# Kernel tuning notes

Hardware: AMD Instinct MI355X
Metric: run time of the kernel (lower is better)

Reference implementation:

```python
import jax, jax.numpy as jnp
import numpy as np

B, C, D, H, W = 2, 128, 32, 64, 64  # ch_in=128, shurink=0 -> Cs = ch_out = C
Cs = C


def setup_inputs() -> dict:
    key = jax.random.key(0)
    ks = jax.random.split(key, 9)
    std = 1.0 / np.sqrt(C).astype(np.float32)
    x = jax.random.normal(ks[0], (B, C, D, H, W), jnp.float32)
    Wk = jax.random.normal(ks[1], (Cs, C), jnp.float32) * std
    bk = jax.random.normal(ks[2], (Cs,), jnp.float32) * std
    Wq = jax.random.normal(ks[3], (Cs, C), jnp.float32) * std
    bq = jax.random.normal(ks[4], (Cs,), jnp.float32) * std
    Wv = jax.random.normal(ks[5], (Cs, C), jnp.float32) * std
    bv = jax.random.normal(ks[6], (Cs,), jnp.float32) * std
    Wo = jax.random.normal(ks[7], (C, Cs), jnp.float32) * (1.0 / np.sqrt(Cs).astype(np.float32))
    bo = jax.random.normal(ks[8], (C,), jnp.float32) * std
    return {"x": x, "Wk": Wk, "bk": bk, "Wq": Wq, "bq": bq, "Wv": Wv, "bv": bv, "Wo": Wo, "bo": bo}


def reference(x, Wk, bk, Wq, bq, Wv, bv, Wo, bo):
    # 1x1x1 Conv3d == per-voxel linear over channels
    def proj(Wt, bt):
        return jnp.einsum('bcdhw,oc->bodhw', x, Wt) + bt[None, :, None, None, None]

    K = proj(Wk, bk)  # [B,Cs,D,H,W]
    Q = proj(Wq, bq)
    V = proj(Wv, bv)

    scale = 1.0 / jnp.sqrt(jnp.asarray(Cs, x.dtype))
    # per-pixel depth attention: scores[b,h,w,i,j] = sum_c K[b,c,i,h,w] * Q[b,c,j,h,w]
    scores = jnp.einsum('bcihw,bcjhw->bhwij', K, Q) * scale
    # torch softmax dim=1 on [N,D,D] == key-position axis i (axis=-2 here)
    A = jax.nn.softmax(scores, axis=-2)
    # a[b,c,j,h,w] = sum_i V[b,c,i,h,w] * A[b,h,w,i,j]  (== bmm(V, A))
    a = jnp.einsum('bcihw,bhwij->bcjhw', V, A)
    out = jnp.einsum('bcjhw,oc->bojhw', a, Wo) + bo[None, :, None, None, None]
    return x + out  # atten_factor = 1
```

## Files before the change

kernel.cpp:

```cpp
#include <hip/hip_runtime.h>

typedef _Float16 f16x8 __attribute__((ext_vector_type(8)));
typedef _Float16 f16x4 __attribute__((ext_vector_type(4)));
typedef float    f32x4 __attribute__((ext_vector_type(4)));

#define MFMA(a,b,c) __builtin_amdgcn_mfma_f32_16x16x32_f16((a),(b),(c),0,0,0)


__global__ __launch_bounds__(128) void prep_kernel(
    const float* __restrict__ Wk, const float* __restrict__ bk,
    const float* __restrict__ Wq, const float* __restrict__ bq,
    const float* __restrict__ Wv, const float* __restrict__ bv,
    const float* __restrict__ Wo, const float* __restrict__ bo,
    _Float16* __restrict__ wh, float* __restrict__ bf) {
  __shared__ float shK[128], shO[128];
  const int o = blockIdx.x;
  const int c = threadIdx.x;
  const float scale = 0.08838834764831844f;
  shK[c] = Wk[c*128 + o];
  shO[c] = Wo[o*128 + c];
  __syncthreads();
  float aM = 0.f, aV = 0.f, tK = 0.f, bV = 0.f;
  for (int m = 0; m < 128; ++m) {
    aM += shK[m] * Wq[m*128 + c];
    aV += shO[m] * Wv[m*128 + c];
    tK += shK[m] * bq[m];
    bV += shO[m] * bv[m];
  }
  wh[o*128 + c]         = (_Float16)(aM * scale);
  wh[16384 + o*128 + c] = (_Float16)aV;
  if (c == 0) { bf[o] = tK * scale; bf[128 + o] = bV + bo[o]; }
}

__device__ __forceinline__ f16x4 cvt4(f32x4 v, f32x4 b) {
  f16x4 r;
  r[0] = (_Float16)(v[0] + b[0]); r[1] = (_Float16)(v[1] + b[1]);
  r[2] = (_Float16)(v[2] + b[2]); r[3] = (_Float16)(v[3] + b[3]);
  return r;
}
__device__ __forceinline__ f16x4 cvt4z(f32x4 v) {
  f16x4 r;
  r[0] = (_Float16)v[0]; r[1] = (_Float16)v[1];
  r[2] = (_Float16)v[2]; r[3] = (_Float16)v[3];
  return r;
}

__device__ __forceinline__ int xsw(int row, int col ) {
  return ((row << 8) | (col << 1)) ^ (((row ^ (row >> 3) ^ (row >> 5)) & 7) << 4);
}

__global__ __launch_bounds__(1024, 4) void attn_kernel(
    const float* __restrict__ x, const _Float16* __restrict__ wh,
    const float* __restrict__ bfp, float* __restrict__ out) {
  __shared__ __align__(16) char lds[151552];
  char* XtB = lds;
  char* YtB = lds + 65536;
  _Float16* At = (_Float16*)(lds + 131072);

  const int tid  = threadIdx.x;
  const int lane = tid & 63;
  const int wv   = tid >> 6;
  const int quad = lane >> 4;
  const int l15  = lane & 15;

  const int bid = blockIdx.x;
  const int g = (bid & ~15) | ((bid & 7) << 1) | ((bid >> 3) & 1);
  const int b   = g >> 9;
  const int rem = g & 511;
  const int h   = rem >> 3;
  const int wg  = rem & 7;
  const size_t pbase = (size_t)b * 16777216u + (size_t)(h*64 + wg*8);
  const f32x4 zz = {0.f, 0.f, 0.f, 0.f};

  const int c4 = tid & 31;
  const int dd = tid >> 5;
  f32x4 v[4][2];
  {
    const float* xg = x + pbase + (size_t)c4*4*131072 + (size_t)dd*4096;
#pragma unroll
    for (int r = 0; r < 4; ++r)
#pragma unroll
      for (int i = 0; i < 2; ++i)
        v[r][i] = *(const f32x4*)(xg + (size_t)r*131072 + i*4);
  }

  const int mi = wv & 7, ni = wv >> 3;
  f16x8 wm[4];
#pragma unroll
  for (int kk = 0; kk < 4; ++kk)
    wm[kk] = *(const f16x8*)(wh + (mi*16 + l15)*128 + kk*32 + quad*8);
  const f32x4 t4 = *(const f32x4*)(bfp + mi*16 + quad*4);

#pragma unroll
  for (int i = 0; i < 2; ++i)
#pragma unroll
    for (int p = 0; p < 4; ++p) {
      f16x4 t;
#pragma unroll
      for (int r = 0; r < 4; ++r) t[r] = (_Float16)v[r][i][p];
      *(f16x4*)(XtB + xsw(dd*8 + i*4 + p, c4*4)) = t;
    }
  __syncthreads();

  {
    f32x4 aY[8] = {zz, zz, zz, zz, zz, zz, zz, zz};
#pragma unroll
    for (int kk = 0; kk < 4; ++kk) {
      const int co = kk*32 + quad*8;
#pragma unroll
      for (int nt = 0; nt < 8; ++nt) {
        const f16x8 bfv = *(const f16x8*)(XtB + xsw(ni*128 + nt*16 + l15, co));
        aY[nt] = MFMA(wm[kk], bfv, aY[nt]);
      }
    }
#pragma unroll
    for (int nt = 0; nt < 8; ++nt)
      *(f16x4*)(YtB + xsw(ni*128 + nt*16 + l15, mi*16 + quad*4)) = cvt4(aY[nt], t4);
  }
  __syncthreads();

  {
    const int p = wv & 7, tj = wv >> 3;
    f32x4 aS[2] = {zz, zz};
#pragma unroll
    for (int kk = 0; kk < 4; ++kk) {
      const int co = kk*32 + quad*8;
      const f16x8 by = *(const f16x8*)(YtB + xsw((tj*16 + l15)*8 + p, co));
#pragma unroll
      for (int ti = 0; ti < 2; ++ti) {
        const f16x8 ak = *(const f16x8*)(XtB + xsw((ti*16 + l15)*8 + p, co));
        aS[ti] = MFMA(ak, by, aS[ti]);
      }
    }
    float mx = aS[0][0];
#pragma unroll
    for (int r = 1; r < 4; ++r) mx = fmaxf(mx, aS[0][r]);
#pragma unroll
    for (int r = 0; r < 4; ++r) mx = fmaxf(mx, aS[1][r]);
    mx = fmaxf(mx, __shfl_xor(mx, 16));
    mx = fmaxf(mx, __shfl_xor(mx, 32));
    float e[2][4];
    float den = 0.f;
#pragma unroll
    for (int ti = 0; ti < 2; ++ti)
#pragma unroll
      for (int r = 0; r < 4; ++r) { e[ti][r] = __expf(aS[ti][r] - mx); den += e[ti][r]; }
    den += __shfl_xor(den, 16);
    den += __shfl_xor(den, 32);
    const float rr = 1.0f / den;
#pragma unroll
    for (int ti = 0; ti < 2; ++ti) {
      f16x4 av;
#pragma unroll
      for (int r = 0; r < 4; ++r) av[r] = (_Float16)(e[ti][r] * rr);
      *(f16x4*)(At + (p*32 + tj*16 + l15)*40 + ti*16 + quad*4) = av;
    }
  }
  __syncthreads();

  f16x8 wp[4];
  {
#pragma unroll
    for (int kk = 0; kk < 4; ++kk)
      wp[kk] = *(const f16x8*)(wh + 16384 + (mi*16 + l15)*128 + kk*32 + quad*8);
    const int p = wv & 7, mg = wv >> 3;
    f16x8 bA[2];
#pragma unroll
    for (int tj = 0; tj < 2; ++tj)
      bA[tj] = *(const f16x8*)(At + (p*32 + tj*16 + l15)*40 + quad*8);
#pragma unroll
    for (int t2 = 0; t2 < 4; ++t2) {
      const int ms = mg*4 + t2;
      f16x8 ax;
#pragma unroll
      for (int jj = 0; jj < 8; ++jj)
        ax[jj] = *(const _Float16*)(XtB + xsw((quad*8 + jj)*8 + p, ms*16 + l15));
#pragma unroll
      for (int tj = 0; tj < 2; ++tj) {
        const f32x4 aU = MFMA(ax, bA[tj], zz);
        *(f16x4*)(YtB + xsw((tj*16 + l15)*8 + p, ms*16 + quad*4)) = cvt4z(aU);
      }
    }
  }
  __syncthreads();

  {
    const int oi = wv & 7, mg6 = wv >> 3;
    f32x4 acc[8] = {zz, zz, zz, zz, zz, zz, zz, zz};
#pragma unroll
    for (int kk = 0; kk < 4; ++kk) {
      const int co = kk*32 + quad*8;
#pragma unroll
      for (int mt = 0; mt < 8; ++mt) {
        const f16x8 av = *(const f16x8*)(YtB + xsw((mg6*8 + mt)*16 + l15, co));
        acc[mt] = MFMA(av, wp[kk], acc[mt]);
      }
    }
    const int o = oi*16 + l15;
    const float bb = bfp[128 + o];
    float* outp = out + pbase + (size_t)o*131072;
#pragma unroll
    for (int mt = 0; mt < 8; ++mt) {
      const int vox0 = (mg6*8 + mt)*16 + quad*4;
      const int d = vox0 >> 3;
      f32x4 vv;
#pragma unroll
      for (int r = 0; r < 4; ++r)
        vv[r] = acc[mt][r] + bb +
                (float)*(const _Float16*)(XtB + xsw(vox0 + r, o));
      *(f32x4*)(outp + (size_t)d*4096 + (vox0 & 7)) = vv;
    }
  }
}

extern "C" void kernel_launch(void* const* d_in, const int* in_sizes, int n_in,
                              void* d_out, int out_size, void* d_ws, size_t ws_size,
                              hipStream_t stream) {
  const float* x  = (const float*)d_in[0];
  const float* Wk = (const float*)d_in[1];
  const float* bk = (const float*)d_in[2];
  const float* Wq = (const float*)d_in[3];
  const float* bq = (const float*)d_in[4];
  const float* Wv = (const float*)d_in[5];
  const float* bv = (const float*)d_in[6];
  const float* Wo = (const float*)d_in[7];
  const float* bo = (const float*)d_in[8];
  float* out = (float*)d_out;
  _Float16* wh = (_Float16*)d_ws;
  float* bf = (float*)((char*)d_ws + 65536);

  prep_kernel<<<dim3(128), dim3(128), 0, stream>>>(Wk, bk, Wq, bq, Wv, bv, Wo, bo, wh, bf);
  attn_kernel<<<dim3(1024), dim3(1024), 0, stream>>>(x, wh, bf, out);
}
```

Before: 347.4 us.

## Process two 8-pixel tiles per block, prefetching the second tile's input during the first

Halves the grid so each block handles 16 w-positions as two sequential passes. The second tile's x data is loaded into registers before the first pass starts, so its global load latency overlaps the first pass's compute. Weight fragments and biases are loaded once and reused across both passes. The cost is higher register pressure from holding the prefetched tile, fewer blocks (512 on the GPU), and dropping the previous block-index swizzle.

```diff
diff --git a/kernel.cpp b/kernel.cpp
--- a/kernel.cpp
+++ b/kernel.cpp
@@ -49,6 +49,126 @@
   return ((row << 8) | (col << 1)) ^ (((row ^ (row >> 3) ^ (row >> 5)) & 7) << 4);
 }
 
+__device__ __forceinline__ void half_pass(
+    char* XtB, char* YtB, _Float16* At,
+    const _Float16* __restrict__ wh, const float* __restrict__ bfp,
+    float* __restrict__ out, size_t pbaseh,
+    int wv, int quad, int l15, const f16x8 (&wm)[4], f32x4 t4, float bb) {
+  const f32x4 zz = {0.f, 0.f, 0.f, 0.f};
+  const int mi = wv & 7, ni = wv >> 3;
+  __syncthreads();
+
+  {
+    f32x4 aY[8] = {zz, zz, zz, zz, zz, zz, zz, zz};
+#pragma unroll
+    for (int kk = 0; kk < 4; ++kk) {
+      const int co = kk*32 + quad*8;
+#pragma unroll
+      for (int nt = 0; nt < 8; ++nt) {
+        const f16x8 bfv = *(const f16x8*)(XtB + xsw(ni*128 + nt*16 + l15, co));
+        aY[nt] = MFMA(wm[kk], bfv, aY[nt]);
+      }
+    }
+#pragma unroll
+    for (int nt = 0; nt < 8; ++nt)
+      *(f16x4*)(YtB + xsw(ni*128 + nt*16 + l15, mi*16 + quad*4)) = cvt4(aY[nt], t4);
+  }
+  __syncthreads();
+
+  {
+    const int p = wv & 7, tj = wv >> 3;
+    f32x4 aS[2] = {zz, zz};
+#pragma unroll
+    for (int kk = 0; kk < 4; ++kk) {
+      const int co = kk*32 + quad*8;
+      const f16x8 by = *(const f16x8*)(YtB + xsw((tj*16 + l15)*8 + p, co));
+#pragma unroll
+      for (int ti = 0; ti < 2; ++ti) {
+        const f16x8 ak = *(const f16x8*)(XtB + xsw((ti*16 + l15)*8 + p, co));
+        aS[ti] = MFMA(ak, by, aS[ti]);
+      }
+    }
+    float mx = aS[0][0];
+#pragma unroll
+    for (int r = 1; r < 4; ++r) mx = fmaxf(mx, aS[0][r]);
+#pragma unroll
+    for (int r = 0; r < 4; ++r) mx = fmaxf(mx, aS[1][r]);
+    mx = fmaxf(mx, __shfl_xor(mx, 16));
+    mx = fmaxf(mx, __shfl_xor(mx, 32));
+    float e[2][4];
+    float den = 0.f;
+#pragma unroll
+    for (int ti = 0; ti < 2; ++ti)
+#pragma unroll
+      for (int r = 0; r < 4; ++r) { e[ti][r] = __expf(aS[ti][r] - mx); den += e[ti][r]; }
+    den += __shfl_xor(den, 16);
+    den += __shfl_xor(den, 32);
+    const float rr = 1.0f / den;
+#pragma unroll
+    for (int ti = 0; ti < 2; ++ti) {
+      f16x4 av;
+#pragma unroll
+      for (int r = 0; r < 4; ++r) av[r] = (_Float16)(e[ti][r] * rr);
+      *(f16x4*)(At + (p*32 + tj*16 + l15)*40 + ti*16 + quad*4) = av;
+    }
+  }
+  __syncthreads();
+
+  f16x8 wp[4];
+  {
+#pragma unroll
+    for (int kk = 0; kk < 4; ++kk)
+      wp[kk] = *(const f16x8*)(wh + 16384 + (mi*16 + l15)*128 + kk*32 + quad*8);
+    const int p = wv & 7, mg = wv >> 3;
+    f16x8 bA[2];
+#pragma unroll
+    for (int tj = 0; tj < 2; ++tj)
+      bA[tj] = *(const f16x8*)(At + (p*32 + tj*16 + l15)*40 + quad*8);
+#pragma unroll
+    for (int t2 = 0; t2 < 4; ++t2) {
+      const int ms = mg*4 + t2;
+      f16x8 ax;
+#pragma unroll
+      for (int jj = 0; jj < 8; ++jj)
+        ax[jj] = *(const _Float16*)(XtB + xsw((quad*8 + jj)*8 + p, ms*16 + l15));
+#pragma unroll
+      for (int tj = 0; tj < 2; ++tj) {
+        const f32x4 aU = MFMA(ax, bA[tj], zz);
+        *(f16x4*)(YtB + xsw((tj*16 + l15)*8 + p, ms*16 + quad*4)) = cvt4z(aU);
+      }
+    }
+  }
+  __syncthreads();
+
+  {
+    const int oi = wv & 7, mg6 = wv >> 3;
+    f32x4 acc[8] = {zz, zz, zz, zz, zz, zz, zz, zz};
+#pragma unroll
+    for (int kk = 0; kk < 4; ++kk) {
+      const int co = kk*32 + quad*8;
+#pragma unroll
+      for (int mt = 0; mt < 8; ++mt) {
+        const f16x8 av = *(const f16x8*)(YtB + xsw((mg6*8 + mt)*16 + l15, co));
+        acc[mt] = MFMA(av, wp[kk], acc[mt]);
+      }
+    }
+    const int o = oi*16 + l15;
+    float* outp = out + pbaseh + (size_t)o*131072;
+#pragma unroll
+    for (int mt = 0; mt < 8; ++mt) {
+      const int vox0 = (mg6*8 + mt)*16 + quad*4;
+      const int d = vox0 >> 3;
+      f32x4 vv;
+#pragma unroll
+      for (int r = 0; r < 4; ++r)
+        vv[r] = acc[mt][r] + bb +
+                (float)*(const _Float16*)(XtB + xsw(vox0 + r, o));
+      *(f32x4*)(outp + (size_t)d*4096 + (vox0 & 7)) = vv;
+    }
+  }
+  __syncthreads();
+}
+
 __global__ __launch_bounds__(1024, 4) void attn_kernel(
     const float* __restrict__ x, const _Float16* __restrict__ wh,
     const float* __restrict__ bfp, float* __restrict__ out) {
@@ -64,32 +184,29 @@
   const int l15  = lane & 15;
 
   const int bid = blockIdx.x;
-  const int g = (bid & ~15) | ((bid & 7) << 1) | ((bid >> 3) & 1);
-  const int b   = g >> 9;
-  const int rem = g & 511;
-  const int h   = rem >> 3;
-  const int wg  = rem & 7;
-  const size_t pbase = (size_t)b * 16777216u + (size_t)(h*64 + wg*8);
-  const f32x4 zz = {0.f, 0.f, 0.f, 0.f};
+  const int b   = bid >> 8;
+  const int rem = bid & 255;
+  const int h   = rem >> 2;
+  const int w16 = rem & 3;
+  const size_t pbase = (size_t)b * 16777216u + (size_t)(h*64 + w16*16);
 
   const int c4 = tid & 31;
   const int dd = tid >> 5;
-  f32x4 v[4][2];
-  {
-    const float* xg = x + pbase + (size_t)c4*4*131072 + (size_t)dd*4096;
-#pragma unroll
-    for (int r = 0; r < 4; ++r)
-#pragma unroll
-      for (int i = 0; i < 2; ++i)
-        v[r][i] = *(const f32x4*)(xg + (size_t)r*131072 + i*4);
-  }
-
-  const int mi = wv & 7, ni = wv >> 3;
+  const float* xg = x + pbase + (size_t)c4*4*131072 + (size_t)dd*4096;
+  f32x4 vA[4][2];
+#pragma unroll
+  for (int r = 0; r < 4; ++r)
+#pragma unroll
+    for (int i = 0; i < 2; ++i)
+      vA[r][i] = *(const f32x4*)(xg + (size_t)r*131072 + i*4);
+
+  const int mi = wv & 7;
   f16x8 wm[4];
 #pragma unroll
   for (int kk = 0; kk < 4; ++kk)
     wm[kk] = *(const f16x8*)(wh + (mi*16 + l15)*128 + kk*32 + quad*8);
   const f32x4 t4 = *(const f32x4*)(bfp + mi*16 + quad*4);
+  const float bb = bfp[128 + (wv & 7)*16 + l15];
 
 #pragma unroll
   for (int i = 0; i < 2; ++i)
@@ -97,120 +214,30 @@
     for (int p = 0; p < 4; ++p) {
       f16x4 t;
 #pragma unroll
-      for (int r = 0; r < 4; ++r) t[r] = (_Float16)v[r][i][p];
+      for (int r = 0; r < 4; ++r) t[r] = (_Float16)vA[r][i][p];
       *(f16x4*)(XtB + xsw(dd*8 + i*4 + p, c4*4)) = t;
     }
-  __syncthreads();
-
-  {
-    f32x4 aY[8] = {zz, zz, zz, zz, zz, zz, zz, zz};
-#pragma unroll
-    for (int kk = 0; kk < 4; ++kk) {
-      const int co = kk*32 + quad*8;
-#pragma unroll
-      for (int nt = 0; nt < 8; ++nt) {
-        const f16x8 bfv = *(const f16x8*)(XtB + xsw(ni*128 + nt*16 + l15, co));
-        aY[nt] = MFMA(wm[kk], bfv, aY[nt]);
-      }
-    }
-#pragma unroll
-    for (int nt = 0; nt < 8; ++nt)
-      *(f16x4*)(YtB + xsw(ni*128 + nt*16 + l15, mi*16 + quad*4)) = cvt4(aY[nt], t4);
-  }
-  __syncthreads();
-
-  {
-    const int p = wv & 7, tj = wv >> 3;
-    f32x4 aS[2] = {zz, zz};
-#pragma unroll
-    for (int kk = 0; kk < 4; ++kk) {
-      const int co = kk*32 + quad*8;
-      const f16x8 by = *(const f16x8*)(YtB + xsw((tj*16 + l15)*8 + p, co));
-#pragma unroll
-      for (int ti = 0; ti < 2; ++ti) {
-        const f16x8 ak = *(const f16x8*)(XtB + xsw((ti*16 + l15)*8 + p, co));
-        aS[ti] = MFMA(ak, by, aS[ti]);
-      }
-    }
-    float mx = aS[0][0];
-#pragma unroll
-    for (int r = 1; r < 4; ++r) mx = fmaxf(mx, aS[0][r]);
-#pragma unroll
-    for (int r = 0; r < 4; ++r) mx = fmaxf(mx, aS[1][r]);
-    mx = fmaxf(mx, __shfl_xor(mx, 16));
-    mx = fmaxf(mx, __shfl_xor(mx, 32));
-    float e[2][4];
-    float den = 0.f;
-#pragma unroll
-    for (int ti = 0; ti < 2; ++ti)
-#pragma unroll
-      for (int r = 0; r < 4; ++r) { e[ti][r] = __expf(aS[ti][r] - mx); den += e[ti][r]; }
-    den += __shfl_xor(den, 16);
-    den += __shfl_xor(den, 32);
-    const float rr = 1.0f / den;
-#pragma unroll
-    for (int ti = 0; ti < 2; ++ti) {
-      f16x4 av;
-#pragma unroll
-      for (int r = 0; r < 4; ++r) av[r] = (_Float16)(e[ti][r] * rr);
-      *(f16x4*)(At + (p*32 + tj*16 + l15)*40 + ti*16 + quad*4) = av;
-    }
-  }
-  __syncthreads();
-
-  f16x8 wp[4];
-  {
-#pragma unroll
-    for (int kk = 0; kk < 4; ++kk)
-      wp[kk] = *(const f16x8*)(wh + 16384 + (mi*16 + l15)*128 + kk*32 + quad*8);
-    const int p = wv & 7, mg = wv >> 3;
-    f16x8 bA[2];
-#pragma unroll
-    for (int tj = 0; tj < 2; ++tj)
-      bA[tj] = *(const f16x8*)(At + (p*32 + tj*16 + l15)*40 + quad*8);
-#pragma unroll
-    for (int t2 = 0; t2 < 4; ++t2) {
-      const int ms = mg*4 + t2;
-      f16x8 ax;
-#pragma unroll
-      for (int jj = 0; jj < 8; ++jj)
-        ax[jj] = *(const _Float16*)(XtB + xsw((quad*8 + jj)*8 + p, ms*16 + l15));
-#pragma unroll
-      for (int tj = 0; tj < 2; ++tj) {
-        const f32x4 aU = MFMA(ax, bA[tj], zz);
-        *(f16x4*)(YtB + xsw((tj*16 + l15)*8 + p, ms*16 + quad*4)) = cvt4z(aU);
-      }
-    }
-  }
-  __syncthreads();
-
-  {
-    const int oi = wv & 7, mg6 = wv >> 3;
-    f32x4 acc[8] = {zz, zz, zz, zz, zz, zz, zz, zz};
-#pragma unroll
-    for (int kk = 0; kk < 4; ++kk) {
-      const int co = kk*32 + quad*8;
-#pragma unroll
-      for (int mt = 0; mt < 8; ++mt) {
-        const f16x8 av = *(const f16x8*)(YtB + xsw((mg6*8 + mt)*16 + l15, co));
-        acc[mt] = MFMA(av, wp[kk], acc[mt]);
-      }
-    }
-    const int o = oi*16 + l15;
-    const float bb = bfp[128 + o];
-    float* outp = out + pbase + (size_t)o*131072;
-#pragma unroll
-    for (int mt = 0; mt < 8; ++mt) {
-      const int vox0 = (mg6*8 + mt)*16 + quad*4;
-      const int d = vox0 >> 3;
-      f32x4 vv;
-#pragma unroll
-      for (int r = 0; r < 4; ++r)
-        vv[r] = acc[mt][r] + bb +
-                (float)*(const _Float16*)(XtB + xsw(vox0 + r, o));
-      *(f32x4*)(outp + (size_t)d*4096 + (vox0 & 7)) = vv;
-    }
-  }
+
+  f32x4 vB[4][2];
+#pragma unroll
+  for (int r = 0; r < 4; ++r)
+#pragma unroll
+    for (int i = 0; i < 2; ++i)
+      vB[r][i] = *(const f32x4*)(xg + (size_t)r*131072 + 8 + i*4);
+
+  half_pass(XtB, YtB, At, wh, bfp, out, pbase, wv, quad, l15, wm, t4, bb);
+
+#pragma unroll
+  for (int i = 0; i < 2; ++i)
+#pragma unroll
+    for (int p = 0; p < 4; ++p) {
+      f16x4 t;
+#pragma unroll
+      for (int r = 0; r < 4; ++r) t[r] = (_Float16)vB[r][i][p];
+      *(f16x4*)(XtB + xsw(dd*8 + i*4 + p, c4*4)) = t;
+    }
+
+  half_pass(XtB, YtB, At, wh, bfp, out, pbase + 8, wv, quad, l15, wm, t4, bb);
 }
 
 extern "C" void kernel_launch(void* const* d_in, const int* in_sizes, int n_in,
@@ -230,5 +257,5 @@
   float* bf = (float*)((char*)d_ws + 65536);
 
   prep_kernel<<<dim3(128), dim3(128), 0, stream>>>(Wk, bk, Wq, bq, Wv, bv, Wo, bo, wh, bf);
-  attn_kernel<<<dim3(1024), dim3(1024), 0, stream>>>(x, wh, bf, out);
-}
+  attn_kernel<<<dim3(512), dim3(1024), 0, stream>>>(x, wh, bf, out);
+}
```

Measured after the change: 545.5 us. 1.57x slower.
